# Optimization experiments

Hardware: AMD Instinct MI355X
Metric: run time of the kernel (lower is better)

Reference implementation:

```python
import jax, jax.numpy as jnp
import numpy as np

N_EMBD = 1024
EXPAND = 2
D_STATE = 16
D_CONV = 4
D_INNER = N_EMBD * EXPAND
DT_RANK = 1  # d_state//16 if >1 else 1, with d_state=16 -> 1


def setup_inputs() -> dict:
    key = jax.random.key(0)
    ks = jax.random.split(key, 8)
    s = 0.02
    x = jax.random.normal(ks[0], (4, 2048, N_EMBD), dtype=jnp.float32)
    in_proj_w = jax.random.normal(ks[1], (N_EMBD, 2 * D_INNER), dtype=jnp.float32) * s
    conv_w = jax.random.normal(ks[2], (D_INNER, 1, D_CONV), dtype=jnp.float32) * s  # depthwise (O,I/g,K)
    conv_b = jax.random.normal(ks[3], (D_INNER,), dtype=jnp.float32) * s
    x_proj_w = jax.random.normal(ks[4], (D_INNER, DT_RANK + 2 * D_STATE), dtype=jnp.float32) * s
    dt_proj_w = jax.random.normal(ks[5], (DT_RANK, D_INNER), dtype=jnp.float32) * s
    dt_proj_b = jax.random.normal(ks[6], (D_INNER,), dtype=jnp.float32) * s
    A_log = jnp.tile(jnp.log(jnp.arange(1, D_STATE + 1, dtype=jnp.float32)), (D_INNER, 1))
    D = jnp.ones((D_INNER,), dtype=jnp.float32)
    out_proj_w = jax.random.normal(ks[7], (D_INNER, N_EMBD), dtype=jnp.float32) * s
    return {"x": x, "in_proj_w": in_proj_w, "conv_w": conv_w, "conv_b": conv_b,
            "x_proj_w": x_proj_w, "dt_proj_w": dt_proj_w, "dt_proj_b": dt_proj_b,
            "A_log": A_log, "D": D, "out_proj_w": out_proj_w}


def _mamba_forward(x, in_proj_w, conv_w, conv_b, x_proj_w, dt_proj_w, dt_proj_b, A_log, D, out_proj_w):
    Bsz, L, _ = x.shape
    d_inner = D.shape[0]
    n_state = A_log.shape[1]
    d_conv = conv_w.shape[-1]
    dt_rank = x_proj_w.shape[1] - 2 * n_state

    xr = x @ in_proj_w                      # [B,L,2*d_inner]
    x_ssm, res = jnp.split(xr, 2, axis=-1)  # each [B,L,d_inner]

    # depthwise causal conv: torch pads both sides by d_conv-1 then truncates to L,
    # equivalent to left-pad d_conv-1 only
    xc = x_ssm.transpose(0, 2, 1)           # [B,d_inner,L]
    xc = jax.lax.conv_general_dilated(
        xc, conv_w, window_strides=(1,), padding=[(d_conv - 1, 0)],
        dimension_numbers=("NCH", "OIH", "NCH"), feature_group_count=d_inner)
    xc = xc + conv_b[None, :, None]
    x_ssm = jax.nn.silu(xc.transpose(0, 2, 1))  # [B,L,d_inner]

    x_dbl = x_ssm @ x_proj_w                 # [B,L,dt_rank+2*n]
    dlt = x_dbl[..., :dt_rank]
    Bv = x_dbl[..., dt_rank:dt_rank + n_state]
    Cv = x_dbl[..., dt_rank + n_state:]
    delta = jax.nn.softplus(dlt @ dt_proj_w + dt_proj_b)  # [B,L,d_inner]

    A = -jnp.exp(A_log)                      # [d_inner,n]

    # time-major for scan
    xt = x_ssm.transpose(1, 0, 2)            # [L,B,d_inner]
    dtm = delta.transpose(1, 0, 2)           # [L,B,d_inner]
    Btm = Bv.transpose(1, 0, 2)              # [L,B,n]
    Ctm = Cv.transpose(1, 0, 2)              # [L,B,n]

    def step(h, inp):
        xt_, dt_, bt_, ct_ = inp
        A_bar = jnp.exp(dt_[..., None] * A)                         # [B,d_inner,n]
        h = A_bar * h + (bt_[:, None, :] * dt_[..., None]) * xt_[..., None]
        y = jnp.einsum("bdn,bn->bd", h, ct_) + D * xt_
        return h, y

    h0 = jnp.zeros((Bsz, d_inner, n_state), dtype=x.dtype)
    _, ys = jax.lax.scan(step, h0, (xt, dtm, Btm, Ctm))  # ys [L,B,d_inner]
    y = ys.transpose(1, 0, 2)                            # [B,L,d_inner]

    out = (y * jax.nn.silu(res)) @ out_proj_w            # [B,L,n_embd]
    return out


def reference(x, in_proj_w, conv_w, conv_b, x_proj_w, dt_proj_w, dt_proj_b, A_log, D, out_proj_w):
    return _mamba_forward(x, in_proj_w, conv_w, conv_b, x_proj_w, dt_proj_w, dt_proj_b, A_log, D, out_proj_w)
```

## Files before the change

### kernel.cpp

```cpp
#include <hip/hip_runtime.h>
#include <hip/hip_bf16.h>
#include <math.h>

#define SEQLEN 2048
#define NROWS  8192
#define DIN    2048
#define CHUNK  64
#define GCH    32

typedef __attribute__((ext_vector_type(8))) short short8;
typedef __attribute__((ext_vector_type(4))) float floatx4;

__device__ __forceinline__ float silu_f(float z) { return z / (1.f + __expf(-z)); }
__device__ __forceinline__ float bfbits2f(unsigned short u) {
  return __uint_as_float(((unsigned int)u) << 16);
}

__device__ __forceinline__ void gld_lds16(const void* gptr, void* lptr) {
  __builtin_amdgcn_global_load_lds((__attribute__((address_space(1))) unsigned int*)gptr,
                                   (__attribute__((address_space(3))) unsigned int*)lptr,
                                   16, 0, 0);
}

template <int BM>
__global__ __launch_bounds__(512) void gemm256(const __hip_bfloat16* __restrict__ A,
                                               const __hip_bfloat16* __restrict__ Bt,
                                               float* __restrict__ C,
                                               __hip_bfloat16* __restrict__ Cb,
                                               __hip_bfloat16* __restrict__ Gb,
                                               int N, int K) {
  constexpr int ABUF   = BM * 32;
  constexpr int ABYTES = ABUF * 2;
  constexpr int FM     = BM / 32;
  __shared__ unsigned short As[4 * ABUF];
  __shared__ unsigned short Bs[4 * 8192];
  const int tid  = threadIdx.x;
  const int lane = tid & 63;
  const int quad = lane >> 4;
  const int l15  = lane & 15;
  const int wv   = tid >> 6;
  const int wm   = wv >> 2;
  const int wn   = wv & 3;
  const int row0 = blockIdx.y * BM;
  const int col0 = blockIdx.x * 256;
  const int NT   = K >> 5;

  const int c0 = tid, c1 = 512 + tid;
  const int r0s = c0 >> 2, j0 = (c0 & 3) ^ ((r0s >> 1) & 3);
  const int r1s = c1 >> 2, j1 = (c1 & 3) ^ ((r1s >> 1) & 3);
  const __hip_bfloat16* a0p = A + (size_t)(row0 + r0s) * K + j0 * 8;
  const __hip_bfloat16* a1p = A + (size_t)(row0 + r1s) * K + j1 * 8;
  const __hip_bfloat16* b0p = Bt + (size_t)(col0 + r0s) * K + j0 * 8;
  const __hip_bfloat16* b1p = Bt + (size_t)(col0 + r1s) * K + j1 * 8;
  const int ldst0 = (wv * 64) * 16;
  const int ldst1 = (512 + wv * 64) * 16;

  const int swz   = (quad ^ ((l15 >> 1) & 3)) << 3;
  const int abase = (wm * (BM / 2) + l15) * 32 + swz;
  const int bbase = (wn * 64 + l15) * 32 + swz;

  floatx4 acc[FM][4] = {};

  if constexpr (BM == 256) {
    gld_lds16(a0p,      (char*)As + ldst0);
    gld_lds16(a1p,      (char*)As + ldst1);
    gld_lds16(b0p,      (char*)Bs + ldst0);
    gld_lds16(b1p,      (char*)Bs + ldst1);
    gld_lds16(a0p + 32, (char*)As + ABYTES + ldst0);
    gld_lds16(a1p + 32, (char*)As + ABYTES + ldst1);
    gld_lds16(b0p + 32, (char*)Bs + 16384 + ldst0);
    gld_lds16(b1p + 32, (char*)Bs + 16384 + ldst1);
    asm volatile("s_waitcnt vmcnt(4)" ::: "memory");
  } else {
    gld_lds16(a0p,      (char*)As + ldst0);
    gld_lds16(b0p,      (char*)Bs + ldst0);
    gld_lds16(b1p,      (char*)Bs + ldst1);
    gld_lds16(a0p + 32, (char*)As + ABYTES + ldst0);
    gld_lds16(b0p + 32, (char*)Bs + 16384 + ldst0);
    gld_lds16(b1p + 32, (char*)Bs + 16384 + ldst1);
    asm volatile("s_waitcnt vmcnt(3)" ::: "memory");
  }
  __builtin_amdgcn_s_barrier();
  __builtin_amdgcn_sched_barrier(0);

  for (int t = 0; t < NT; t++) {
    const unsigned short* Ab = As + (t & 3) * ABUF;
    const unsigned short* Bb = Bs + (t & 3) * 8192;
    const int t2     = t + 2;
    const int kof2   = t2 * 32;
    const int dbufA2 = (t2 & 3) * ABYTES;
    const int dbufB2 = (t2 & 3) * 16384;

    if constexpr (BM == 256) {
      short8 a[4], b[4];

#pragma unroll
      for (int m = 0; m < 4; m++) a[m] = *(const short8*)&Ab[abase + m * 512];
#pragma unroll
      for (int n = 0; n < 4; n++) b[n] = *(const short8*)&Bb[bbase + n * 512];
      if (t2 < NT) {
        gld_lds16(a0p + kof2, (char*)As + dbufA2 + ldst0);
        gld_lds16(a1p + kof2, (char*)As + dbufA2 + ldst1);
      }
      __builtin_amdgcn_s_barrier();
      asm volatile("s_waitcnt lgkmcnt(0)" ::: "memory");
      __builtin_amdgcn_sched_barrier(0);
      __builtin_amdgcn_s_setprio(1);
#pragma unroll
      for (int m = 0; m < 4; m++)
#pragma unroll
        for (int n = 0; n < 4; n++)
          acc[m][n] = __builtin_amdgcn_mfma_f32_16x16x32_bf16(a[m], b[n], acc[m][n], 0, 0, 0);
      __builtin_amdgcn_s_setprio(0);
      __builtin_amdgcn_sched_barrier(0);
      __builtin_amdgcn_s_barrier();

#pragma unroll
      for (int m = 0; m < 4; m++) a[m] = *(const short8*)&Ab[abase + (4 + m) * 512];
      if (t2 < NT) {
        gld_lds16(b0p + kof2, (char*)Bs + dbufB2 + ldst0);
        gld_lds16(b1p + kof2, (char*)Bs + dbufB2 + ldst1);
      }
      __builtin_amdgcn_s_barrier();
      asm volatile("s_waitcnt lgkmcnt(0)" ::: "memory");
      __builtin_amdgcn_sched_barrier(0);
      __builtin_amdgcn_s_setprio(1);
#pragma unroll
      for (int m = 0; m < 4; m++)
#pragma unroll
        for (int n = 0; n < 4; n++)
          acc[4 + m][n] = __builtin_amdgcn_mfma_f32_16x16x32_bf16(a[m], b[n], acc[4 + m][n], 0, 0, 0);
      __builtin_amdgcn_s_setprio(0);
      __builtin_amdgcn_sched_barrier(0);

      if (t < NT - 1) {
        if (t >= NT - 2) asm volatile("s_waitcnt vmcnt(0)" ::: "memory");
        else             asm volatile("s_waitcnt vmcnt(4)" ::: "memory");
        __builtin_amdgcn_s_barrier();
        __builtin_amdgcn_sched_barrier(0);
      }
    } else {
      short8 a[4], b[4];
#pragma unroll
      for (int m = 0; m < 4; m++) a[m] = *(const short8*)&Ab[abase + m * 512];
#pragma unroll
      for (int n = 0; n < 4; n++) b[n] = *(const short8*)&Bb[bbase + n * 512];
      if (t2 < NT) {
        gld_lds16(a0p + kof2, (char*)As + dbufA2 + ldst0);
        gld_lds16(b0p + kof2, (char*)Bs + dbufB2 + ldst0);
        gld_lds16(b1p + kof2, (char*)Bs + dbufB2 + ldst1);
      }
      __builtin_amdgcn_s_barrier();
      asm volatile("s_waitcnt lgkmcnt(0)" ::: "memory");
      __builtin_amdgcn_sched_barrier(0);
      __builtin_amdgcn_s_setprio(1);
#pragma unroll
      for (int m = 0; m < 4; m++)
#pragma unroll
        for (int n = 0; n < 4; n++)
          acc[m][n] = __builtin_amdgcn_mfma_f32_16x16x32_bf16(a[m], b[n], acc[m][n], 0, 0, 0);
      __builtin_amdgcn_s_setprio(0);
      __builtin_amdgcn_sched_barrier(0);

      if (t < NT - 1) {
        if (t >= NT - 2) asm volatile("s_waitcnt vmcnt(0)" ::: "memory");
        else             asm volatile("s_waitcnt vmcnt(3)" ::: "memory");
        __builtin_amdgcn_s_barrier();
        __builtin_amdgcn_sched_barrier(0);
      }
    }
  }

  const int Nh = N >> 1;
#pragma unroll
  for (int fm = 0; fm < FM; fm++) {
    int rbase = row0 + wm * (BM / 2) + fm * 16 + quad * 4;
#pragma unroll
    for (int n = 0; n < 4; n++) {
      int col = col0 + wn * 64 + n * 16 + l15;
#pragma unroll
      for (int r = 0; r < 4; r++) {
        float v = acc[fm][n][r];
        if (Cb) {
          if (col < Nh) Cb[(size_t)(rbase + r) * Nh + col] = __float2bfloat16(v);
          else          Gb[(size_t)(rbase + r) * Nh + col - Nh] = __float2bfloat16(silu_f(v));
        } else {
          C[(size_t)(rbase + r) * N + col] = v;
        }
      }
    }
  }
}

__global__ __launch_bounds__(256) void gemm_bf16(const __hip_bfloat16* __restrict__ A,
                                                 const __hip_bfloat16* __restrict__ Bt,
                                                 float* __restrict__ C,
                                                 int M, int N, int K) {
  __shared__ unsigned short As[128 * 64];
  __shared__ unsigned short Bs[128 * 64];
  const int tid  = threadIdx.x;
  const int lane = tid & 63;
  const int quad = lane >> 4;
  const int l15  = lane & 15;
  const int wv   = tid >> 6;
  const int wm   = wv >> 1;
  const int wn   = wv & 1;
  const int row0 = blockIdx.y * 128;
  const int col0 = blockIdx.x * 128;
  const int swz  = l15 & 7;

  floatx4 acc[4][4] = {};

  for (int k0 = 0; k0 < K; k0 += 64) {
#pragma unroll
    for (int i = 0; i < 4; i++) {
      int c = tid + i * 256;
      int r = c >> 3, j = c & 7;
      int js = j ^ (r & 7);
      gld_lds16(A + (size_t)(row0 + r) * K + k0 + js * 8,
                (char*)As + (size_t)(i * 256 + wv * 64) * 16);
      gld_lds16(Bt + (size_t)(col0 + r) * K + k0 + js * 8,
                (char*)Bs + (size_t)(i * 256 + wv * 64) * 16);
    }
    __syncthreads();
#pragma unroll
    for (int ks = 0; ks < 64; ks += 32) {
      const int sj = (((ks >> 3) + quad) ^ swz) << 3;
      short8 a[4], b[4];
#pragma unroll
      for (int t = 0; t < 4; t++) {
        a[t] = *(const short8*)&As[(wm * 64 + t * 16 + l15) * 64 + sj];
        b[t] = *(const short8*)&Bs[(wn * 64 + t * 16 + l15) * 64 + sj];
      }
#pragma unroll
      for (int tm = 0; tm < 4; tm++)
#pragma unroll
        for (int tn = 0; tn < 4; tn++)
          acc[tm][tn] = __builtin_amdgcn_mfma_f32_16x16x32_bf16(a[tm], b[tn], acc[tm][tn], 0, 0, 0);
    }
    __syncthreads();
  }
#pragma unroll
  for (int tm = 0; tm < 4; tm++) {
    int rbase = row0 + wm * 64 + tm * 16 + quad * 4;
#pragma unroll
    for (int tn = 0; tn < 4; tn++) {
      int col = col0 + wn * 64 + tn * 16 + l15;
#pragma unroll
      for (int r = 0; r < 4; r++)
        C[(size_t)(rbase + r) * N + col] = acc[tm][tn][r];
    }
  }
}

__global__ __launch_bounds__(256) void convert_bf16(const float* __restrict__ in,
                                                    __hip_bfloat16* __restrict__ out,
                                                    int n) {
  int i = (blockIdx.x * 256 + threadIdx.x) * 4;
  if (i >= n) return;
  float4 v = *reinterpret_cast<const float4*>(in + i);
  out[i + 0] = __float2bfloat16(v.x);
  out[i + 1] = __float2bfloat16(v.y);
  out[i + 2] = __float2bfloat16(v.z);
  out[i + 3] = __float2bfloat16(v.w);
}

__global__ __launch_bounds__(256) void transpose_bf16(const float* __restrict__ w,
                                                      __hip_bfloat16* __restrict__ wt,
                                                      int K, int N) {
  __shared__ float tile[32][33];
  int n0 = blockIdx.x * 32, k0 = blockIdx.y * 32;
  int tx = threadIdx.x;
#pragma unroll
  for (int i = threadIdx.y; i < 32; i += 8)
    tile[i][tx] = w[(size_t)(k0 + i) * N + n0 + tx];
  __syncthreads();
#pragma unroll
  for (int i = threadIdx.y; i < 32; i += 8)
    wt[(size_t)(n0 + i) * K + k0 + tx] = __float2bfloat16(tile[tx][i]);
}

__global__ __launch_bounds__(256) void pack_xproj(const float* __restrict__ w,
                                                  __hip_bfloat16* __restrict__ wtp) {
  int idx = blockIdx.x * 256 + threadIdx.x;
  int n = idx >> 11;
  int k = idx & 2047;
  int src = (n == 0) ? 0 : ((n >= 4 && n < 36) ? (n - 3) : -1);
  float v = (src >= 0) ? w[(size_t)k * 33 + src] : 0.f;
  wtp[idx] = __float2bfloat16(v);
}

__global__ __launch_bounds__(256) void conv_silu_kernel(const __hip_bfloat16* __restrict__ xssm,
                                                        const float* __restrict__ conv_w,
                                                        const float* __restrict__ conv_b,
                                                        float* __restrict__ x_c,
                                                        __hip_bfloat16* __restrict__ x_cb) {
  int idx = blockIdx.x * blockDim.x + threadIdx.x;
  if (idx >= NROWS * DIN) return;
  int d = idx & (DIN - 1);
  int row = idx >> 11;
  int l = row & (SEQLEN - 1);
  float acc = conv_b[d];
#pragma unroll
  for (int k = 0; k < 4; k++) {
    int ls = l + k - 3;
    if (ls >= 0)
      acc = fmaf(conv_w[d * 4 + k],
                 __bfloat162float(xssm[(size_t)(row + k - 3) * DIN + d]), acc);
  }
  float v = silu_f(acc);
  x_c[idx] = v;
  x_cb[idx] = __float2bfloat16(v);
}

__global__ __launch_bounds__(256) void scan_passA(const float* __restrict__ x_c,
                                                  const float* __restrict__ xd,
                                                  const float* __restrict__ dt_w,
                                                  const float* __restrict__ dt_b,
                                                  float* __restrict__ hend,
                                                  float* __restrict__ sumdelta) {
  const int d = blockIdx.x * 256 + threadIdx.x;
  const int b = blockIdx.y >> 5;
  const int g = blockIdx.y & 31;
  const int ch = b * DIN + d;
  const float dtw = dt_w[d], dtb = dt_b[d];
  float h[16];
#pragma unroll
  for (int n = 0; n < 16; n++) h[n] = 0.f;
  float sd = 0.f;
  const int row = b * SEQLEN + g * CHUNK;
  const float* xdr = xd + (size_t)row * 128;
  const float* xcr = x_c + (size_t)row * DIN + d;
  float dl = xdr[0];
  float4 B0 = *(const float4*)(xdr + 4);
  float4 B1 = *(const float4*)(xdr + 8);
  float4 B2 = *(const float4*)(xdr + 12);
  float4 B3 = *(const float4*)(xdr + 16);
  float xv = *xcr;
  for (int l = 0; l < CHUNK; l++) {
    const int adv = (l < CHUNK - 1) ? 1 : 0;
    const float* xdn = xdr + adv * 128;
    const float* xcn = xcr + adv * DIN;
    float dl_n = xdn[0];
    float4 B0n = *(const float4*)(xdn + 4);
    float4 B1n = *(const float4*)(xdn + 8);
    float4 B2n = *(const float4*)(xdn + 12);
    float4 B3n = *(const float4*)(xdn + 16);
    float xv_n = *xcn;

    float z = fmaf(dl, dtw, dtb);
    float e = __expf(z);
    float denom = 1.f + e;
    float delta = __logf(denom);
    float r = __builtin_amdgcn_rcpf(denom);
    sd += delta;
    float dx = delta * xv;
    float p2 = r * r, p3 = p2 * r, p4 = p2 * p2;
    float b2 = p4 * p4, b3 = b2 * p4;
    h[0]  = fmaf(r,       h[0],  B0.x * dx);
    h[1]  = fmaf(p2,      h[1],  B0.y * dx);
    h[2]  = fmaf(p3,      h[2],  B0.z * dx);
    h[3]  = fmaf(p4,      h[3],  B0.w * dx);
    h[4]  = fmaf(p4 * r,  h[4],  B1.x * dx);
    h[5]  = fmaf(p4 * p2, h[5],  B1.y * dx);
    h[6]  = fmaf(p4 * p3, h[6],  B1.z * dx);
    h[7]  = fmaf(b2,      h[7],  B1.w * dx);
    h[8]  = fmaf(b2 * r,  h[8],  B2.x * dx);
    h[9]  = fmaf(b2 * p2, h[9],  B2.y * dx);
    h[10] = fmaf(b2 * p3, h[10], B2.z * dx);
    h[11] = fmaf(b3,      h[11], B2.w * dx);
    h[12] = fmaf(b3 * r,  h[12], B3.x * dx);
    h[13] = fmaf(b3 * p2, h[13], B3.y * dx);
    h[14] = fmaf(b3 * p3, h[14], B3.z * dx);
    h[15] = fmaf(b3 * p4, h[15], B3.w * dx);

    dl = dl_n; xv = xv_n; B0 = B0n; B1 = B1n; B2 = B2n; B3 = B3n;
    xdr = xdn; xcr = xcn;
  }
  size_t base = ((size_t)g * 8192 + ch) * 16;
#pragma unroll
  for (int n = 0; n < 16; n += 4) {
    float4 hv = {h[n], h[n + 1], h[n + 2], h[n + 3]};
    *reinterpret_cast<float4*>(&hend[base + n]) = hv;
  }
  sumdelta[(size_t)g * 8192 + ch] = sd;
}

__global__ __launch_bounds__(256) void scan_passB(const float* __restrict__ A_log,
                                                  const float* __restrict__ sumdelta,
                                                  const float* __restrict__ hend,
                                                  float* __restrict__ hinit) {
  int t = blockIdx.x * 256 + threadIdx.x;
  int ch = t >> 2, q = t & 3;
  int d = ch & (DIN - 1);
  float4 al = *reinterpret_cast<const float4*>(&A_log[d * 16 + q * 4]);
  const float An0 = -__expf(al.x), An1 = -__expf(al.y),
              An2 = -__expf(al.z), An3 = -__expf(al.w);
  float4 h = {0.f, 0.f, 0.f, 0.f};
#pragma unroll
  for (int g = 0; g < GCH; g++) {
    size_t base = ((size_t)g * 8192 + ch) * 16 + q * 4;
    *reinterpret_cast<float4*>(&hinit[base]) = h;
    float sd = sumdelta[(size_t)g * 8192 + ch];
    float4 he = *reinterpret_cast<const float4*>(&hend[base]);
    h.x = fmaf(__expf(An0 * sd), h.x, he.x);
    h.y = fmaf(__expf(An1 * sd), h.y, he.y);
    h.z = fmaf(__expf(An2 * sd), h.z, he.z);
    h.w = fmaf(__expf(An3 * sd), h.w, he.w);
  }
}

__global__ __launch_bounds__(256) void scan_passC(const float* __restrict__ x_c,
                                                  const float* __restrict__ xd,
                                                  const float* __restrict__ dt_w,
                                                  const float* __restrict__ dt_b,
                                                  const float* __restrict__ Dp,
                                                  const float* __restrict__ hinit,
                                                  const __hip_bfloat16* __restrict__ gate,
                                                  __hip_bfloat16* __restrict__ outg) {
  const int d = blockIdx.x * 256 + threadIdx.x;
  const int b = blockIdx.y >> 5;
  const int g = blockIdx.y & 31;
  const int ch = b * DIN + d;
  const float dtw = dt_w[d], dtb = dt_b[d], Dd = Dp[d];
  float h[16];
  {
    size_t base = ((size_t)g * 8192 + ch) * 16;
#pragma unroll
    for (int n = 0; n < 16; n += 4) {
      float4 hv = *reinterpret_cast<const float4*>(&hinit[base + n]);
      h[n] = hv.x; h[n + 1] = hv.y; h[n + 2] = hv.z; h[n + 3] = hv.w;
    }
  }
  const int row0 = b * SEQLEN + g * CHUNK;
  const float* xdr = xd + (size_t)row0 * 128;
  const float* xcr = x_c + (size_t)row0 * DIN + d;
  const __hip_bfloat16* gtr = gate + (size_t)row0 * DIN + d;
  __hip_bfloat16* otr = outg + (size_t)row0 * DIN + d;
  float dl = xdr[0];
  float4 B0 = *(const float4*)(xdr + 4);
  float4 B1 = *(const float4*)(xdr + 8);
  float4 B2 = *(const float4*)(xdr + 12);
  float4 B3 = *(const float4*)(xdr + 16);
  float4 C0 = *(const float4*)(xdr + 20);
  float4 C1 = *(const float4*)(xdr + 24);
  float4 C2 = *(const float4*)(xdr + 28);
  float4 C3 = *(const float4*)(xdr + 32);
  float xv = *xcr;
  float gv = bfbits2f(*(const unsigned short*)gtr);
  for (int l = 0; l < CHUNK; l++) {
    const int adv = (l < CHUNK - 1) ? 1 : 0;
    const float* xdn = xdr + adv * 128;
    const float* xcn = xcr + adv * DIN;
    const __hip_bfloat16* gtn = gtr + adv * DIN;
    float dl_n = xdn[0];
    float4 B0n = *(const float4*)(xdn + 4);
    float4 B1n = *(const float4*)(xdn + 8);
    float4 B2n = *(const float4*)(xdn + 12);
    float4 B3n = *(const float4*)(xdn + 16);
    float4 C0n = *(const float4*)(xdn + 20);
    float4 C1n = *(const float4*)(xdn + 24);
    float4 C2n = *(const float4*)(xdn + 28);
    float4 C3n = *(const float4*)(xdn + 32);
    float xv_n = *xcn;
    float gv_n = bfbits2f(*(const unsigned short*)gtn);

    float z = fmaf(dl, dtw, dtb);
    float e = __expf(z);
    float denom = 1.f + e;
    float delta = __logf(denom);
    float r = __builtin_amdgcn_rcpf(denom);
    float dx = delta * xv;
    float p2 = r * r, p3 = p2 * r, p4 = p2 * p2;
    float b2 = p4 * p4, b3 = b2 * p4;
    h[0]  = fmaf(r,       h[0],  B0.x * dx);
    h[1]  = fmaf(p2,      h[1],  B0.y * dx);
    h[2]  = fmaf(p3,      h[2],  B0.z * dx);
    h[3]  = fmaf(p4,      h[3],  B0.w * dx);
    h[4]  = fmaf(p4 * r,  h[4],  B1.x * dx);
    h[5]  = fmaf(p4 * p2, h[5],  B1.y * dx);
    h[6]  = fmaf(p4 * p3, h[6],  B1.z * dx);
    h[7]  = fmaf(b2,      h[7],  B1.w * dx);
    h[8]  = fmaf(b2 * r,  h[8],  B2.x * dx);
    h[9]  = fmaf(b2 * p2, h[9],  B2.y * dx);
    h[10] = fmaf(b2 * p3, h[10], B2.z * dx);
    h[11] = fmaf(b3,      h[11], B2.w * dx);
    h[12] = fmaf(b3 * r,  h[12], B3.x * dx);
    h[13] = fmaf(b3 * p2, h[13], B3.y * dx);
    h[14] = fmaf(b3 * p3, h[14], B3.z * dx);
    h[15] = fmaf(b3 * p4, h[15], B3.w * dx);

    float y0 = fmaf(h[0],  C0.x, fmaf(h[1],  C0.y, fmaf(h[2],  C0.z, h[3]  * C0.w)));
    float y1 = fmaf(h[4],  C1.x, fmaf(h[5],  C1.y, fmaf(h[6],  C1.z, h[7]  * C1.w)));
    float y2 = fmaf(h[8],  C2.x, fmaf(h[9],  C2.y, fmaf(h[10], C2.z, h[11] * C2.w)));
    float y3 = fmaf(h[12], C3.x, fmaf(h[13], C3.y, fmaf(h[14], C3.z, h[15] * C3.w)));
    float y = (y0 + y1) + (y2 + y3);
    *(unsigned short*)otr = __bfloat16_as_ushort(__float2bfloat16(fmaf(Dd, xv, y) * gv));

    dl = dl_n; xv = xv_n; gv = gv_n;
    B0 = B0n; B1 = B1n; B2 = B2n; B3 = B3n;
    C0 = C0n; C1 = C1n; C2 = C2n; C3 = C3n;
    xdr = xdn; xcr = xcn; gtr = gtn; otr += adv * DIN;
  }
}

extern "C" void kernel_launch(void* const* d_in, const int* in_sizes, int n_in,
                              void* d_out, int out_size, void* d_ws, size_t ws_size,
                              hipStream_t stream) {
  const float* x         = (const float*)d_in[0];
  const float* in_proj_w = (const float*)d_in[1];
  const float* conv_w    = (const float*)d_in[2];
  const float* conv_b    = (const float*)d_in[3];
  const float* x_proj_w  = (const float*)d_in[4];
  const float* dt_proj_w = (const float*)d_in[5];
  const float* dt_proj_b = (const float*)d_in[6];
  const float* A_log     = (const float*)d_in[7];
  const float* Dp        = (const float*)d_in[8];
  const float* out_proj_w= (const float*)d_in[9];
  float* out = (float*)d_out;

  const size_t MB = 1u << 20;
  char* ws = (char*)d_ws;
  __hip_bfloat16* xb      = (__hip_bfloat16*)(ws);
  float*          xdbl128 = (float*)(ws);
  float*          sumdl   = (float*)(ws + 4 * MB);
  __hip_bfloat16* wtp     = (__hip_bfloat16*)(ws + 5 * MB);
  __hip_bfloat16* wt3     = (__hip_bfloat16*)(ws + 6 * MB);
  __hip_bfloat16* wt1     = (__hip_bfloat16*)(ws + 16 * MB);
  __hip_bfloat16* xssm_bf = (__hip_bfloat16*)(ws + 24 * MB);
  float*          hend    = (float*)(ws + 24 * MB);
  __hip_bfloat16* gate_bf = (__hip_bfloat16*)(ws + 56 * MB);
  float*          x_c     = (float*)(ws + 88 * MB);
  __hip_bfloat16* x_cb    = (__hip_bfloat16*)(ws + 152 * MB);
  __hip_bfloat16* gated   = (__hip_bfloat16*)(ws + 152 * MB);
  float*          hinit   = (float*)(ws + 184 * MB);

  convert_bf16<<<(NROWS * 1024) / 1024, 256, 0, stream>>>(x, xb, NROWS * 1024);
  transpose_bf16<<<dim3(4096 / 32, 1024 / 32), dim3(32, 8), 0, stream>>>(in_proj_w, wt1, 1024, 4096);

  gemm256<256><<<dim3(4096 / 256, NROWS / 256), 512, 0, stream>>>(
      xb, wt1, (float*)nullptr, xssm_bf, gate_bf, 4096, 1024);

  conv_silu_kernel<<<(NROWS * DIN) / 256, 256, 0, stream>>>(xssm_bf, conv_w, conv_b, x_c, x_cb);

  pack_xproj<<<(128 * 2048) / 256, 256, 0, stream>>>(x_proj_w, wtp);
  gemm_bf16<<<dim3(1, NROWS / 128), 256, 0, stream>>>(
      x_cb, wtp, xdbl128, NROWS, 128, 2048);

  scan_passA<<<dim3(DIN / 256, 4 * GCH), 256, 0, stream>>>(x_c, xdbl128, dt_proj_w, dt_proj_b, hend, sumdl);
  scan_passB<<<128, 256, 0, stream>>>(A_log, sumdl, hend, hinit);
  scan_passC<<<dim3(DIN / 256, 4 * GCH), 256, 0, stream>>>(x_c, xdbl128, dt_proj_w, dt_proj_b, Dp, hinit,
                                                           gate_bf, gated);

  transpose_bf16<<<dim3(1024 / 32, 2048 / 32), dim3(32, 8), 0, stream>>>(out_proj_w, wt3, 2048, 1024);

  gemm256<128><<<dim3(1024 / 256, NROWS / 128), 512, 0, stream>>>(
      gated, wt3, out, (__hip_bfloat16*)nullptr, (__hip_bfloat16*)nullptr, 1024, 2048);
}
```

Measured before the change: 465.2 us.

## Add XCD-aware block swizzle, deeper prefetch, and split-K x_proj GEMM

Remaps GEMM block indices so that neighbouring tiles land on the same XCD, which should improve L2 reuse of A and B panels. For the BM=128 out_proj GEMM it deepens the global-to-LDS prefetch from two stages to three, and one barrier is removed from the loop. The narrow x_proj GEMM (N=128) is split four ways along K to raise the block count, followed by a reduce kernel. The cost is an extra kernel launch and partial-sum traffic, plus closer ordering constraints in the pipelined loop.

```diff
diff --git a/kernel.cpp b/kernel.cpp
--- a/kernel.cpp
+++ b/kernel.cpp
@@ -28,7 +28,7 @@
                                                float* __restrict__ C,
                                                __hip_bfloat16* __restrict__ Cb,
                                                __hip_bfloat16* __restrict__ Gb,
-                                               int N, int K) {
+                                               int N, int K, int cgx, int cgy) {
   constexpr int ABUF   = BM * 32;
   constexpr int ABYTES = ABUF * 2;
   constexpr int FM     = BM / 32;
@@ -41,8 +41,16 @@
   const int wv   = tid >> 6;
   const int wm   = wv >> 2;
   const int wn   = wv & 3;
-  const int row0 = blockIdx.y * BM;
-  const int col0 = blockIdx.x * 256;
+
+  const int GX  = gridDim.x;
+  const int lid = blockIdx.y * GX + blockIdx.x;
+  const int xcd = lid & 7;
+  const int seq = lid >> 3;
+  const int cpr = GX / cgx;
+  const int bx  = (xcd % cpr) * cgx + (seq % cgx);
+  const int by  = (xcd / cpr) * cgy + (seq / cgx);
+  const int row0 = by * BM;
+  const int col0 = bx * 256;
   const int NT   = K >> 5;
 
   const int c0 = tid, c1 = 512 + tid;
@@ -71,27 +79,17 @@
     gld_lds16(b0p + 32, (char*)Bs + 16384 + ldst0);
     gld_lds16(b1p + 32, (char*)Bs + 16384 + ldst1);
     asm volatile("s_waitcnt vmcnt(4)" ::: "memory");
-  } else {
-    gld_lds16(a0p,      (char*)As + ldst0);
-    gld_lds16(b0p,      (char*)Bs + ldst0);
-    gld_lds16(b1p,      (char*)Bs + ldst1);
-    gld_lds16(a0p + 32, (char*)As + ABYTES + ldst0);
-    gld_lds16(b0p + 32, (char*)Bs + 16384 + ldst0);
-    gld_lds16(b1p + 32, (char*)Bs + 16384 + ldst1);
-    asm volatile("s_waitcnt vmcnt(3)" ::: "memory");
-  }
-  __builtin_amdgcn_s_barrier();
-  __builtin_amdgcn_sched_barrier(0);
-
-  for (int t = 0; t < NT; t++) {
-    const unsigned short* Ab = As + (t & 3) * ABUF;
-    const unsigned short* Bb = Bs + (t & 3) * 8192;
-    const int t2     = t + 2;
-    const int kof2   = t2 * 32;
-    const int dbufA2 = (t2 & 3) * ABYTES;
-    const int dbufB2 = (t2 & 3) * 16384;
-
-    if constexpr (BM == 256) {
+    __builtin_amdgcn_s_barrier();
+    __builtin_amdgcn_sched_barrier(0);
+
+    for (int t = 0; t < NT; t++) {
+      const unsigned short* Ab = As + (t & 3) * ABUF;
+      const unsigned short* Bb = Bs + (t & 3) * 8192;
+      const int t2    = t + 2;
+      const int kof2  = t2 * 32;
+      const int dbufA2 = (t2 & 3) * ABYTES;
+      const int dbufB2 = (t2 & 3) * 16384;
+
       short8 a[4], b[4];
 
 #pragma unroll
@@ -139,18 +137,39 @@
         __builtin_amdgcn_s_barrier();
         __builtin_amdgcn_sched_barrier(0);
       }
-    } else {
+    }
+  } else {
+#pragma unroll
+    for (int p = 0; p < 3; p++) {
+      const int kof = p * 32;
+      const int dA = p * ABYTES, dB = p * 16384;
+      gld_lds16(a0p + kof, (char*)As + dA + ldst0);
+      gld_lds16(b0p + kof, (char*)Bs + dB + ldst0);
+      gld_lds16(b1p + kof, (char*)Bs + dB + ldst1);
+    }
+    asm volatile("s_waitcnt vmcnt(6)" ::: "memory");
+    __builtin_amdgcn_s_barrier();
+    __builtin_amdgcn_sched_barrier(0);
+
+    for (int t = 0; t < NT; t++) {
+      const unsigned short* Ab = As + (t & 3) * ABUF;
+      const unsigned short* Bb = Bs + (t & 3) * 8192;
+      const int t3     = t + 3;
+      const int kof3   = t3 * 32;
+      const int dbufA3 = (t3 & 3) * ABYTES;
+      const int dbufB3 = (t3 & 3) * 16384;
+
       short8 a[4], b[4];
 #pragma unroll
       for (int m = 0; m < 4; m++) a[m] = *(const short8*)&Ab[abase + m * 512];
 #pragma unroll
       for (int n = 0; n < 4; n++) b[n] = *(const short8*)&Bb[bbase + n * 512];
-      if (t2 < NT) {
-        gld_lds16(a0p + kof2, (char*)As + dbufA2 + ldst0);
-        gld_lds16(b0p + kof2, (char*)Bs + dbufB2 + ldst0);
-        gld_lds16(b1p + kof2, (char*)Bs + dbufB2 + ldst1);
-      }
-      __builtin_amdgcn_s_barrier();
+      __builtin_amdgcn_sched_barrier(0);
+      if (t3 < NT) {
+        gld_lds16(a0p + kof3, (char*)As + dbufA3 + ldst0);
+        gld_lds16(b0p + kof3, (char*)Bs + dbufB3 + ldst0);
+        gld_lds16(b1p + kof3, (char*)Bs + dbufB3 + ldst1);
+      }
       asm volatile("s_waitcnt lgkmcnt(0)" ::: "memory");
       __builtin_amdgcn_sched_barrier(0);
       __builtin_amdgcn_s_setprio(1);
@@ -163,8 +182,9 @@
       __builtin_amdgcn_sched_barrier(0);
 
       if (t < NT - 1) {
-        if (t >= NT - 2) asm volatile("s_waitcnt vmcnt(0)" ::: "memory");
-        else             asm volatile("s_waitcnt vmcnt(3)" ::: "memory");
+        if (t < NT - 3)       asm volatile("s_waitcnt vmcnt(6)" ::: "memory");
+        else if (t == NT - 3) asm volatile("s_waitcnt vmcnt(3)" ::: "memory");
+        else                  asm volatile("s_waitcnt vmcnt(0)" ::: "memory");
         __builtin_amdgcn_s_barrier();
         __builtin_amdgcn_sched_barrier(0);
       }
@@ -194,7 +214,7 @@
 
 __global__ __launch_bounds__(256) void gemm_bf16(const __hip_bfloat16* __restrict__ A,
                                                  const __hip_bfloat16* __restrict__ Bt,
-                                                 float* __restrict__ C,
+                                                 float* __restrict__ Cpart,
                                                  int M, int N, int K) {
   __shared__ unsigned short As[128 * 64];
   __shared__ unsigned short Bs[128 * 64];
@@ -206,12 +226,15 @@
   const int wm   = wv >> 1;
   const int wn   = wv & 1;
   const int row0 = blockIdx.y * 128;
-  const int col0 = blockIdx.x * 128;
+  const int col0 = 0;
+  const int kc   = K / gridDim.x;
+  const int kbeg = blockIdx.x * kc, kend = kbeg + kc;
+  float* Cp = Cpart + (size_t)blockIdx.x * ((size_t)M * N);
   const int swz  = l15 & 7;
 
   floatx4 acc[4][4] = {};
 
-  for (int k0 = 0; k0 < K; k0 += 64) {
+  for (int k0 = kbeg; k0 < kend; k0 += 64) {
 #pragma unroll
     for (int i = 0; i < 4; i++) {
       int c = tid + i * 256;
@@ -248,9 +271,22 @@
       int col = col0 + wn * 64 + tn * 16 + l15;
 #pragma unroll
       for (int r = 0; r < 4; r++)
-        C[(size_t)(rbase + r) * N + col] = acc[tm][tn][r];
-    }
-  }
+        Cp[(size_t)(rbase + r) * N + col] = acc[tm][tn][r];
+    }
+  }
+}
+
+__global__ __launch_bounds__(256) void reduce4(const float* __restrict__ p,
+                                               float* __restrict__ o, int n) {
+  int i = (blockIdx.x * 256 + threadIdx.x) * 4;
+  if (i >= n) return;
+  float4 a = *(const float4*)(p + i);
+  float4 b = *(const float4*)(p + (size_t)n + i);
+  float4 c = *(const float4*)(p + 2 * (size_t)n + i);
+  float4 d = *(const float4*)(p + 3 * (size_t)n + i);
+  float4 r = {(a.x + b.x) + (c.x + d.x), (a.y + b.y) + (c.y + d.y),
+              (a.z + b.z) + (c.z + d.z), (a.w + b.w) + (c.w + d.w)};
+  *(float4*)(o + i) = r;
 }
 
 __global__ __launch_bounds__(256) void convert_bf16(const float* __restrict__ in,
@@ -529,6 +565,7 @@
   __hip_bfloat16* wt1     = (__hip_bfloat16*)(ws + 16 * MB);
   __hip_bfloat16* xssm_bf = (__hip_bfloat16*)(ws + 24 * MB);
   float*          hend    = (float*)(ws + 24 * MB);
+  float*          xpart   = (float*)(ws + 40 * MB);
   __hip_bfloat16* gate_bf = (__hip_bfloat16*)(ws + 56 * MB);
   float*          x_c     = (float*)(ws + 88 * MB);
   __hip_bfloat16* x_cb    = (__hip_bfloat16*)(ws + 152 * MB);
@@ -539,13 +576,14 @@
   transpose_bf16<<<dim3(4096 / 32, 1024 / 32), dim3(32, 8), 0, stream>>>(in_proj_w, wt1, 1024, 4096);
 
   gemm256<256><<<dim3(4096 / 256, NROWS / 256), 512, 0, stream>>>(
-      xb, wt1, (float*)nullptr, xssm_bf, gate_bf, 4096, 1024);
+      xb, wt1, (float*)nullptr, xssm_bf, gate_bf, 4096, 1024, 8, 8);
 
   conv_silu_kernel<<<(NROWS * DIN) / 256, 256, 0, stream>>>(xssm_bf, conv_w, conv_b, x_c, x_cb);
 
   pack_xproj<<<(128 * 2048) / 256, 256, 0, stream>>>(x_proj_w, wtp);
-  gemm_bf16<<<dim3(1, NROWS / 128), 256, 0, stream>>>(
-      x_cb, wtp, xdbl128, NROWS, 128, 2048);
+  gemm_bf16<<<dim3(4, NROWS / 128), 256, 0, stream>>>(
+      x_cb, wtp, xpart, NROWS, 128, 2048);
+  reduce4<<<(NROWS * 128) / 1024, 256, 0, stream>>>(xpart, xdbl128, NROWS * 128);
 
   scan_passA<<<dim3(DIN / 256, 4 * GCH), 256, 0, stream>>>(x_c, xdbl128, dt_proj_w, dt_proj_b, hend, sumdl);
   scan_passB<<<128, 256, 0, stream>>>(A_log, sumdl, hend, hinit);
@@ -555,5 +593,5 @@
   transpose_bf16<<<dim3(1024 / 32, 2048 / 32), dim3(32, 8), 0, stream>>>(out_proj_w, wt3, 2048, 1024);
 
   gemm256<128><<<dim3(1024 / 256, NROWS / 128), 512, 0, stream>>>(
-      gated, wt3, out, (__hip_bfloat16*)nullptr, (__hip_bfloat16*)nullptr, 1024, 2048);
-}
+      gated, wt3, out, (__hip_bfloat16*)nullptr, (__hip_bfloat16*)nullptr, 1024, 2048, 4, 8);
+}
```

Measured after the change: 436.6 us. 6.1% less time.
